# Performance work log

Measured on AMD Instinct MI355X. Metric: run time of the kernel, lower is better.

Reference implementation:

```python
import math
import jax, jax.numpy as jnp
import numpy as np

D_MODEL = 1024
D_FF = 4096
NUM_EXPERTS = 8
TOP_K = 2
CAP_FACTOR = 1.0
AUX_COEF = 0.01
Z_COEF = 0.0


def setup_inputs() -> dict:
    key = jax.random.key(0)
    ks = jax.random.split(key, 6)
    x = jax.random.normal(ks[0], (4, 2048, D_MODEL), dtype=jnp.float32)
    router_w = jax.random.normal(ks[1], (D_MODEL, NUM_EXPERTS), dtype=jnp.float32) / math.sqrt(D_MODEL)
    router_b = jnp.zeros((NUM_EXPERTS,), dtype=jnp.float32)
    w1 = jax.random.normal(ks[2], (NUM_EXPERTS, D_MODEL, D_FF), dtype=jnp.float32) / math.sqrt(D_MODEL)
    w3 = jax.random.normal(ks[3], (NUM_EXPERTS, D_MODEL, D_FF), dtype=jnp.float32) / math.sqrt(D_MODEL)
    w2 = jax.random.normal(ks[4], (NUM_EXPERTS, D_FF, D_MODEL), dtype=jnp.float32) / math.sqrt(D_FF)
    return {"x": x, "router_w": router_w, "router_b": router_b, "w1": w1, "w3": w3, "w2": w2}


def reference(x, router_w, router_b, w1, w3, w2):
    b, s, d = x.shape
    E, k = NUM_EXPERTS, TOP_K
    T = b * s
    x_flat = x.reshape(T, d)

    # ---- router ----
    logits = x_flat @ router_w + router_b                      # [T, E]
    logits_f32 = logits.astype(jnp.float32)
    probs = jax.nn.softmax(logits_f32, axis=-1)                # [T, E]
    topk_p, topk_i = jax.lax.top_k(probs, k)                   # [T, k]
    topk_p = topk_p / jnp.clip(topk_p.sum(-1, keepdims=True), 1e-9)  # normalize_gates
    gate = topk_p.reshape(-1)                                  # [T*k]
    expert_idx = topk_i.reshape(-1)                            # [T*k]

    # ---- aux loss (load balance + z-loss) ----
    importance = probs.mean(axis=0)                            # [E]
    load = jnp.bincount(topk_i[:, 0], length=E).astype(jnp.float32) / T
    lb_loss = (importance * load).sum() * float(E)
    z_loss = jnp.mean(jnp.square(jax.nn.logsumexp(logits_f32, axis=-1)))
    aux_loss = (AUX_COEF * lb_loss + Z_COEF * z_loss).astype(x.dtype)

    # ---- capacity-based dispatch ----
    N = T * k
    cap = max(1, int(math.ceil(CAP_FACTOR * N / E)))
    x_rep = jnp.repeat(x_flat, k, axis=0)                      # [N, d]
    order = jnp.argsort(expert_idx)                            # stable sort by expert
    e_sorted = expert_idx[order]
    x_sorted = x_rep[order]
    g_sorted = gate[order].astype(x.dtype)
    counts = jnp.bincount(e_sorted, length=E)
    starts = jnp.concatenate([jnp.zeros((1,), counts.dtype), jnp.cumsum(counts)[:-1]])
    pos = jnp.arange(N, dtype=counts.dtype) - starts[e_sorted]   # rank within expert group
    keep = pos < cap
    slot = jnp.where(keep, e_sorted * cap + pos, E * cap)      # dropped tokens -> dump row

    buf = jnp.zeros((E * cap + 1, d), dtype=x.dtype).at[slot].set(x_sorted)
    buf = buf[: E * cap].reshape(E, cap, d)                    # [E, C, d]

    # ---- grouped SwiGLU experts ----
    h = jax.nn.silu(jnp.einsum('ecd,edf->ecf', buf, w1)) * jnp.einsum('ecd,edf->ecf', buf, w3)
    y = jnp.einsum('ecf,efd->ecd', h, w2).reshape(E * cap, d)

    # ---- combine ----
    gathered = y[jnp.minimum(slot, E * cap - 1)]
    out_sorted = jnp.where(keep[:, None], gathered, 0.0) * g_sorted[:, None]
    inv = jnp.argsort(order)
    out = out_sorted[inv].reshape(T, k, d).sum(axis=1)
    return out.reshape(b, s, d), aux_loss
```

## Files before the change

### kernel.cpp

```cpp
#include <hip/hip_runtime.h>
#include <hip/hip_bf16.h>
#include <math.h>

constexpr int kT    = 8192;
constexpr int kD    = 1024;
constexpr int kF    = 4096;
constexpr int kE    = 8;
constexpr int kN    = kT * 2;
constexpr int kCap  = 2048;
constexpr int kECap = kE * kCap;

typedef __attribute__((ext_vector_type(8))) short bf16x8;
typedef __attribute__((ext_vector_type(4))) float f32x4;

__device__ __forceinline__ void gload16(const __hip_bfloat16* g, __hip_bfloat16* l) {
  auto gp = (const __attribute__((address_space(1))) __hip_bfloat16*)g;
  auto lp = (__attribute__((address_space(3))) __hip_bfloat16*)l;
  __builtin_amdgcn_global_load_lds((const __attribute__((address_space(1))) void*)gp,
                                   (__attribute__((address_space(3))) void*)lp,
                                   16, 0, 0);
}

#define SYNC_VM(N) do { __builtin_amdgcn_sched_barrier(0); \
  asm volatile("s_waitcnt vmcnt(" #N ")" ::: "memory"); \
  __builtin_amdgcn_s_barrier(); \
  asm volatile("" ::: "memory"); } while (0)

__global__ void init_kernel(int* token_of) {
  int i = blockIdx.x * 256 + threadIdx.x;
  if (i < kECap) token_of[i] = -1;
}

__global__ __launch_bounds__(256)
void transpose64_kernel(const float* __restrict__ srcA, const float* __restrict__ srcB,
                        __hip_bfloat16* __restrict__ dstA, __hip_bfloat16* __restrict__ dstB,
                        int R, int C) {
  __shared__ float tile[64][65];
  const int zz = blockIdx.z;
  const int e = zz & 7;
  const float* src = (zz < 8) ? srcA : srcB;
  __hip_bfloat16* dst = (zz < 8) ? dstA : dstB;
  const size_t mat = (size_t)R * C;
  const float* s = src + (size_t)e * mat;
  __hip_bfloat16* d = dst + (size_t)e * mat;
  const int c0 = blockIdx.x * 64, r0 = blockIdx.y * 64;
  const int tid = threadIdx.x;

  const int lr = tid >> 4, lc4 = (tid & 15) * 4;
#pragma unroll
  for (int p = 0; p < 4; ++p) {
    int r = p * 16 + lr;
    float4 v = *(const float4*)(s + (size_t)(r0 + r) * C + c0 + lc4);
    tile[r][lc4] = v.x; tile[r][lc4 + 1] = v.y; tile[r][lc4 + 2] = v.z; tile[r][lc4 + 3] = v.w;
  }
  __syncthreads();

  const int c = tid >> 2, rc = (tid & 3) * 16;
  union { __hip_bfloat16 h[16]; bf16x8 v[2]; } o;
#pragma unroll
  for (int i = 0; i < 16; ++i) o.h[i] = __float2bfloat16(tile[rc + i][c]);
  __hip_bfloat16* drow = d + (size_t)(c0 + c) * R + r0 + rc;
  *(bf16x8*)drow = o.v[0];
  *(bf16x8*)(drow + 8) = o.v[1];
}

__global__ __launch_bounds__(256)
void router_kernel(const float* __restrict__ x, const float* __restrict__ rw,
                   const float* __restrict__ rb, int* __restrict__ e_idx,
                   float* __restrict__ gates, float* __restrict__ probs_out) {
  int t = blockIdx.x * 4 + (threadIdx.x >> 6);
  int lane = threadIdx.x & 63;
  const float* xr = x + (size_t)t * kD;
  float acc[8];
#pragma unroll
  for (int e = 0; e < 8; ++e) acc[e] = 0.f;
  for (int i = 0; i < kD / 256; ++i) {
    int d = i * 256 + lane * 4;
    float4 xv = *(const float4*)(xr + d);
#pragma unroll
    for (int j = 0; j < 4; ++j) {
      float xs = (j == 0) ? xv.x : (j == 1) ? xv.y : (j == 2) ? xv.z : xv.w;
      const float4* w4 = (const float4*)(rw + (size_t)(d + j) * 8);
      float4 wa = w4[0], wb = w4[1];
      acc[0] += xs * wa.x; acc[1] += xs * wa.y; acc[2] += xs * wa.z; acc[3] += xs * wa.w;
      acc[4] += xs * wb.x; acc[5] += xs * wb.y; acc[6] += xs * wb.z; acc[7] += xs * wb.w;
    }
  }
#pragma unroll
  for (int off = 32; off >= 1; off >>= 1) {
#pragma unroll
    for (int e = 0; e < 8; ++e) acc[e] += __shfl_xor(acc[e], off);
  }
  if (lane == 0) {
    float l[8], m = -1e30f;
#pragma unroll
    for (int e = 0; e < 8; ++e) { l[e] = acc[e] + rb[e]; m = fmaxf(m, l[e]); }
    float p[8], s = 0.f;
#pragma unroll
    for (int e = 0; e < 8; ++e) { p[e] = __expf(l[e] - m); s += p[e]; }
    float inv = 1.f / s;
#pragma unroll
    for (int e = 0; e < 8; ++e) p[e] *= inv;
    int i1 = 0;
#pragma unroll
    for (int e = 1; e < 8; ++e) if (p[e] > p[i1]) i1 = e;
    int i2 = (i1 == 0) ? 1 : 0;
#pragma unroll
    for (int e = 0; e < 8; ++e) if (e != i1 && e != i2 && p[e] > p[i2]) i2 = e;
    float den = fmaxf(p[i1] + p[i2], 1e-9f);
    e_idx[2 * t] = i1; e_idx[2 * t + 1] = i2;
    gates[2 * t] = p[i1] / den; gates[2 * t + 1] = p[i2] / den;
    float4* po = (float4*)(probs_out + (size_t)t * 8);
    po[0] = make_float4(p[0], p[1], p[2], p[3]);
    po[1] = make_float4(p[4], p[5], p[6], p[7]);
  }
}

__global__ __launch_bounds__(1024)
void aux_kernel(const float* __restrict__ probs, const int* __restrict__ e_idx,
                float* __restrict__ aux_out) {
  int tid = threadIdx.x, lane = tid & 63, wave = tid >> 6;
  float imp[8];
  int cnt[8];
#pragma unroll
  for (int e = 0; e < 8; ++e) { imp[e] = 0.f; cnt[e] = 0; }
  for (int t = tid; t < kT; t += 1024) {
    const float4* p4 = (const float4*)(probs + (size_t)t * 8);
    float4 a = p4[0], b = p4[1];
    imp[0] += a.x; imp[1] += a.y; imp[2] += a.z; imp[3] += a.w;
    imp[4] += b.x; imp[5] += b.y; imp[6] += b.z; imp[7] += b.w;
    ++cnt[e_idx[2 * t] & 7];
  }
#pragma unroll
  for (int off = 32; off >= 1; off >>= 1) {
#pragma unroll
    for (int e = 0; e < 8; ++e) {
      imp[e] += __shfl_xor(imp[e], off);
      cnt[e] += __shfl_xor(cnt[e], off);
    }
  }
  __shared__ float simp[16][8];
  __shared__ int scnt[16][8];
  if (lane == 0) {
#pragma unroll
    for (int e = 0; e < 8; ++e) { simp[wave][e] = imp[e]; scnt[wave][e] = cnt[e]; }
  }
  __syncthreads();
  if (tid == 0) {
    float lb = 0.f;
    for (int e = 0; e < 8; ++e) {
      float I = 0.f; int C = 0;
      for (int w = 0; w < 16; ++w) { I += simp[w][e]; C += scnt[w][e]; }
      lb += (I / (float)kT) * ((float)C / (float)kT);
    }
    aux_out[0] = 0.01f * lb * (float)kE;
  }
}

__global__ __launch_bounds__(256)
void rank_kernel(const int* __restrict__ e_idx, int* __restrict__ pos) {
  int e = blockIdx.x;
  __shared__ int wave_sum[4];
  __shared__ int running;
  int tid = threadIdx.x, lane = tid & 63, wave = tid >> 6;
  if (tid == 0) running = 0;
  __syncthreads();
  for (int base = 0; base < kN; base += 256) {
    int i = base + tid;
    bool f = (e_idx[i] == e);
    unsigned long long m = __ballot(f);
    int wpre = __popcll(m & ((1ull << lane) - 1ull));
    if (lane == 0) wave_sum[wave] = __popcll(m);
    __syncthreads();
    int woff = 0;
    for (int w = 0; w < wave; ++w) woff += wave_sum[w];
    int r = running;
    if (f) pos[i] = r + woff + wpre;
    __syncthreads();
    if (tid == 0) running = r + wave_sum[0] + wave_sum[1] + wave_sum[2] + wave_sum[3];
    __syncthreads();
  }
}

__global__ __launch_bounds__(256)
void scatter_kernel(const int* __restrict__ e_idx, const int* __restrict__ pos,
                    int* __restrict__ slot_of, int* __restrict__ token_of) {
  int i = blockIdx.x * 256 + threadIdx.x;
  if (i >= kN) return;
  int p = pos[i];
  if (p < kCap) {
    int slot = e_idx[i] * kCap + p;
    slot_of[i] = slot;
    token_of[slot] = i >> 1;
  } else {
    slot_of[i] = -1;
  }
}

struct __attribute__((aligned(8))) bf16x4s { __hip_bfloat16 v[4]; };

__global__ __launch_bounds__(64)
void gather_kernel(const float* __restrict__ x, const int* __restrict__ token_of,
                   __hip_bfloat16* __restrict__ buf) {
  int slot = blockIdx.x, lane = threadIdx.x;
  int t = token_of[slot];
  __hip_bfloat16* br = buf + (size_t)slot * kD;
  if (t >= 0) {
    const float* xr = x + (size_t)t * kD;
#pragma unroll
    for (int j = 0; j < 4; ++j) {
      int dd = (j * 64 + lane) * 4;
      float4 v = *(const float4*)(xr + dd);
      bf16x4s o;
      o.v[0] = __float2bfloat16(v.x); o.v[1] = __float2bfloat16(v.y);
      o.v[2] = __float2bfloat16(v.z); o.v[3] = __float2bfloat16(v.w);
      *(bf16x4s*)(br + dd) = o;
    }
  } else {
    bf16x4s z;
    z.v[0] = z.v[1] = z.v[2] = z.v[3] = __float2bfloat16(0.f);
#pragma unroll
    for (int j = 0; j < 4; ++j) *(bf16x4s*)(br + (j * 64 + lane) * 4) = z;
  }
}

__global__ __launch_bounds__(512, 2)
void gemm1_kernel(const __hip_bfloat16* __restrict__ Abase,
                  const __hip_bfloat16* __restrict__ W1t,
                  const __hip_bfloat16* __restrict__ W3t,
                  __hip_bfloat16* __restrict__ H) {
  constexpr int K = kD;
  constexpr int NT = K / 64;
  const int e = blockIdx.z, mt = blockIdx.y, ft = blockIdx.x;
  const int tid = threadIdx.x, lane = tid & 63, wave = tid >> 6;
  const int wr = wave >> 1, wc = wave & 1;
  const int frow = lane & 15, fk = lane >> 4;

  const __hip_bfloat16* A  = Abase + (size_t)(e * kCap + mt * 256) * K;
  const __hip_bfloat16* B1 = W1t + ((size_t)e * kF + ft * 128) * K;
  const __hip_bfloat16* B3 = W3t + ((size_t)e * kF + ft * 128) * K;

  extern __shared__ __hip_bfloat16 lds[];

  f32x4 accU[4][4], accV[4][4];
#pragma unroll
  for (int m = 0; m < 4; ++m)
#pragma unroll
    for (int n = 0; n < 4; ++n) {
      accU[m][n] = (f32x4){0.f, 0.f, 0.f, 0.f};
      accV[m][n] = (f32x4){0.f, 0.f, 0.f, 0.f};
    }

  auto stageA = [&](int t, int b) {
#pragma unroll
    for (int j = 0; j < 4; ++j) {
      int c = j * 128 + wc * 64 + lane;
      int rl = c >> 3, s = c & 7;
      const __hip_bfloat16* g = A + (size_t)(wr * 64 + rl) * K + t * 64 + (s ^ (rl & 7)) * 8;
      gload16(g, &lds[b * 32768 + wr * 4096 + (j * 128 + wc * 64) * 8]);
    }
  };
  auto stageB1 = [&](int t, int b) {
#pragma unroll
    for (int j = 0; j < 2; ++j) {
      int c = j * 256 + wr * 64 + lane;
      int rl = c >> 3, s = c & 7;
      const __hip_bfloat16* g = B1 + (size_t)(wc * 64 + rl) * K + t * 64 + (s ^ (rl & 7)) * 8;
      gload16(g, &lds[b * 32768 + 16384 + wc * 4096 + (j * 256 + wr * 64) * 8]);
    }
  };
  auto stageB3 = [&](int t, int b) {
#pragma unroll
    for (int j = 0; j < 2; ++j) {
      int c = j * 256 + wr * 64 + lane;
      int rl = c >> 3, s = c & 7;
      const __hip_bfloat16* g = B3 + (size_t)(wc * 64 + rl) * K + t * 64 + (s ^ (rl & 7)) * 8;
      gload16(g, &lds[b * 32768 + 16384 + 8192 + wc * 4096 + (j * 256 + wr * 64) * 8]);
    }
  };
  auto phase = [&](int b, f32x4 (&ac)[4][4], bf16x8 (&af)[4][2], int broff, bool loadA) {
    if (loadA) {
#pragma unroll
      for (int m = 0; m < 4; ++m)
#pragma unroll
        for (int h = 0; h < 2; ++h) {
          int row = wr * 64 + m * 16 + frow;
          af[m][h] = *(const bf16x8*)&lds[b * 32768 + row * 64 + ((h * 4 + fk) ^ (row & 7)) * 8];
        }
    }
    bf16x8 bf[4][2];
#pragma unroll
    for (int n = 0; n < 4; ++n)
#pragma unroll
      for (int h = 0; h < 2; ++h) {
        int row = broff + wc * 64 + n * 16 + frow;
        bf[n][h] = *(const bf16x8*)&lds[b * 32768 + 16384 + row * 64 + ((h * 4 + fk) ^ (row & 7)) * 8];
      }
    __builtin_amdgcn_s_setprio(1);
#pragma unroll
    for (int m = 0; m < 4; ++m)
#pragma unroll
      for (int n = 0; n < 4; ++n)
#pragma unroll
        for (int h = 0; h < 2; ++h)
          ac[m][n] = __builtin_amdgcn_mfma_f32_16x16x32_bf16(af[m][h], bf[n][h], ac[m][n], 0, 0, 0);
    __builtin_amdgcn_s_setprio(0);
    __builtin_amdgcn_sched_barrier(0);
  };

  stageA(0, 0); stageB1(0, 0); stageB3(0, 0);

  for (int t = 0; t < NT; ++t) {
    const int b = t & 1, nb = b ^ 1;
    const bool nx = (t + 1 < NT);
    SYNC_VM(2);
    if (nx) stageA(t + 1, nb);
    bf16x8 af[4][2];
    phase(b, accU, af, 0, true);
    if (nx) { SYNC_VM(4); } else { SYNC_VM(0); }
    if (nx) stageB1(t + 1, nb);
    phase(b, accV, af, 128, false);
    if (nx) stageB3(t + 1, nb);
  }

  __hip_bfloat16* Ht = H + (size_t)(e * kCap + mt * 256) * kF + ft * 128;
#pragma unroll
  for (int m = 0; m < 4; ++m)
#pragma unroll
    for (int n = 0; n < 4; ++n)
#pragma unroll
      for (int r = 0; r < 4; ++r) {
        int row = wr * 64 + m * 16 + fk * 4 + r;
        int col = wc * 64 + n * 16 + frow;
        float u = accU[m][n][r], v = accV[m][n][r];
        float hval = (u / (1.f + __expf(-u))) * v;
        Ht[(size_t)row * kF + col] = __float2bfloat16(hval);
      }
}

__global__ __launch_bounds__(512, 2)
void gemm2_kernel(const __hip_bfloat16* __restrict__ Hbase,
                  const __hip_bfloat16* __restrict__ W2t,
                  __hip_bfloat16* __restrict__ Y) {
  constexpr int K = kF;
  constexpr int NT = K / 64;
  const int e = blockIdx.z, mt = blockIdx.y, nt = blockIdx.x;
  const int tid = threadIdx.x, lane = tid & 63, wave = tid >> 6;
  const int wr = wave >> 2, wc = wave & 3;
  const int frow = lane & 15, fk = lane >> 4;

  const __hip_bfloat16* A = Hbase + (size_t)(e * kCap + mt * 256) * K;
  const __hip_bfloat16* B = W2t + ((size_t)e * kD + nt * 256) * K;

  extern __shared__ __hip_bfloat16 lds[];

  f32x4 acc[2][4][4];
#pragma unroll
  for (int p = 0; p < 2; ++p)
#pragma unroll
    for (int m = 0; m < 4; ++m)
#pragma unroll
      for (int n = 0; n < 4; ++n) acc[p][m][n] = (f32x4){0.f, 0.f, 0.f, 0.f};

  auto stageB = [&](int t, int b) {
#pragma unroll
    for (int j = 0; j < 4; ++j) {
      int c = j * 128 + wr * 64 + lane;
      int rl = c >> 3, s = c & 7;
      const __hip_bfloat16* g = B + (size_t)(wc * 64 + rl) * K + t * 64 + (s ^ (rl & 7)) * 8;
      gload16(g, &lds[b * 32768 + 16384 + wc * 4096 + (j * 128 + wr * 64) * 8]);
    }
  };
  auto stageA = [&](int t, int p, int b) {
    int q = 2 * wr + p;
#pragma unroll
    for (int j = 0; j < 2; ++j) {
      int c = j * 256 + wc * 64 + lane;
      int rl = c >> 3, s = c & 7;
      const __hip_bfloat16* g = A + (size_t)(q * 64 + rl) * K + t * 64 + (s ^ (rl & 7)) * 8;
      gload16(g, &lds[b * 32768 + q * 4096 + (j * 256 + wc * 64) * 8]);
    }
  };
  auto phase = [&](int b, int p, f32x4 (&ac)[4][4], bf16x8 (&bf)[4][2], bool loadB) {
    bf16x8 a[4][2];
#pragma unroll
    for (int m = 0; m < 4; ++m)
#pragma unroll
      for (int h = 0; h < 2; ++h) {
        int row = wr * 128 + p * 64 + m * 16 + frow;
        a[m][h] = *(const bf16x8*)&lds[b * 32768 + row * 64 + ((h * 4 + fk) ^ (row & 7)) * 8];
      }
    if (loadB) {
#pragma unroll
      for (int n = 0; n < 4; ++n)
#pragma unroll
        for (int h = 0; h < 2; ++h) {
          int row = wc * 64 + n * 16 + frow;
          bf[n][h] = *(const bf16x8*)&lds[b * 32768 + 16384 + row * 64 + ((h * 4 + fk) ^ (row & 7)) * 8];
        }
    }
    __builtin_amdgcn_s_setprio(1);
#pragma unroll
    for (int m = 0; m < 4; ++m)
#pragma unroll
      for (int n = 0; n < 4; ++n)
#pragma unroll
        for (int h = 0; h < 2; ++h)
          ac[m][n] = __builtin_amdgcn_mfma_f32_16x16x32_bf16(a[m][h], bf[n][h], ac[m][n], 0, 0, 0);
    __builtin_amdgcn_s_setprio(0);
    __builtin_amdgcn_sched_barrier(0);
  };

  stageB(0, 0); stageA(0, 0, 0); stageA(0, 1, 0);

  for (int t = 0; t < NT; ++t) {
    const int b = t & 1, nb = b ^ 1;
    const bool nx = (t + 1 < NT);
    SYNC_VM(2);
    if (nx) stageB(t + 1, nb);
    bf16x8 bf[4][2];
    phase(b, 0, acc[0], bf, true);
    if (nx) { SYNC_VM(4); } else { SYNC_VM(0); }
    if (nx) stageA(t + 1, 0, nb);
    phase(b, 1, acc[1], bf, false);
    if (nx) stageA(t + 1, 1, nb);
  }

  __hip_bfloat16* Yt = Y + (size_t)(e * kCap + mt * 256) * kD + nt * 256;
#pragma unroll
  for (int p = 0; p < 2; ++p)
#pragma unroll
    for (int m = 0; m < 4; ++m)
#pragma unroll
      for (int n = 0; n < 4; ++n)
#pragma unroll
        for (int r = 0; r < 4; ++r) {
          int row = wr * 128 + p * 64 + m * 16 + fk * 4 + r;
          int col = wc * 64 + n * 16 + frow;
          Yt[(size_t)row * kD + col] = __float2bfloat16(acc[p][m][n][r]);
        }
}

__global__ __launch_bounds__(256)
void combine_kernel(const __hip_bfloat16* __restrict__ Y, const int* __restrict__ slot_of,
                    const float* __restrict__ gates, float* __restrict__ out) {
  int t = blockIdx.x;
  int dd = threadIdx.x * 4;
  int s0 = slot_of[2 * t], s1 = slot_of[2 * t + 1];
  float g0 = gates[2 * t], g1 = gates[2 * t + 1];
  float4 r = {0.f, 0.f, 0.f, 0.f};
  if (s0 >= 0) {
    bf16x4s v = *(const bf16x4s*)(Y + (size_t)s0 * kD + dd);
    r.x += g0 * __bfloat162float(v.v[0]); r.y += g0 * __bfloat162float(v.v[1]);
    r.z += g0 * __bfloat162float(v.v[2]); r.w += g0 * __bfloat162float(v.v[3]);
  }
  if (s1 >= 0) {
    bf16x4s v = *(const bf16x4s*)(Y + (size_t)s1 * kD + dd);
    r.x += g1 * __bfloat162float(v.v[0]); r.y += g1 * __bfloat162float(v.v[1]);
    r.z += g1 * __bfloat162float(v.v[2]); r.w += g1 * __bfloat162float(v.v[3]);
  }
  *(float4*)(out + (size_t)t * kD + dd) = r;
}

extern "C" void kernel_launch(void* const* d_in, const int* in_sizes, int n_in,
                              void* d_out, int out_size, void* d_ws, size_t ws_size,
                              hipStream_t stream) {
  (void)in_sizes; (void)n_in; (void)out_size; (void)ws_size;
  const float* x  = (const float*)d_in[0];
  const float* rw = (const float*)d_in[1];
  const float* rb = (const float*)d_in[2];
  const float* w1 = (const float*)d_in[3];
  const float* w3 = (const float*)d_in[4];
  const float* w2 = (const float*)d_in[5];
  float* out = (float*)d_out;

  char* base = (char*)d_ws;
  size_t off = 0;
  auto alloc = [&](size_t bytes) -> char* {
    char* r = base + off;
    off += (bytes + 255) & ~(size_t)255;
    return r;
  };
  __hip_bfloat16* w1t = (__hip_bfloat16*)alloc((size_t)kE * kF * kD * 2);
  __hip_bfloat16* w3t = (__hip_bfloat16*)alloc((size_t)kE * kF * kD * 2);
  __hip_bfloat16* w2t = (__hip_bfloat16*)alloc((size_t)kE * kD * kF * 2);
  __hip_bfloat16* buf = (__hip_bfloat16*)alloc((size_t)kECap * kD * 2);
  __hip_bfloat16* h   = (__hip_bfloat16*)alloc((size_t)kECap * kF * 2);
  __hip_bfloat16* y   = (__hip_bfloat16*)alloc((size_t)kECap * kD * 2);
  int*   e_idx    = (int*)alloc((size_t)kN * 4);
  float* gates    = (float*)alloc((size_t)kN * 4);
  int*   pos      = (int*)alloc((size_t)kN * 4);
  int*   slot_of  = (int*)alloc((size_t)kN * 4);
  int*   token_of = (int*)alloc((size_t)kECap * 4);
  float* probs    = (float*)alloc((size_t)kT * 8 * 4);

  init_kernel<<<kECap / 256, 256, 0, stream>>>(token_of);
  router_kernel<<<kT / 4, 256, 0, stream>>>(x, rw, rb, e_idx, gates, probs);
  aux_kernel<<<1, 1024, 0, stream>>>(probs, e_idx, out + (size_t)kT * kD);
  rank_kernel<<<kE, 256, 0, stream>>>(e_idx, pos);
  scatter_kernel<<<kN / 256, 256, 0, stream>>>(e_idx, pos, slot_of, token_of);
  gather_kernel<<<kECap, 64, 0, stream>>>(x, token_of, buf);
  transpose64_kernel<<<dim3(kF / 64, kD / 64, 16), 256, 0, stream>>>(w1, w3, w1t, w3t, kD, kF);
  gemm1_kernel<<<dim3(kF / 128, kCap / 256, kE), 512, 131072, stream>>>(buf, w1t, w3t, h);
  transpose64_kernel<<<dim3(kD / 64, kF / 64, 8), 256, 0, stream>>>(w2, w2, w2t, w2t, kF, kD);
  gemm2_kernel<<<dim3(kD / 256, kCap / 256, kE), 512, 131072, stream>>>(h, w2t, y);
  combine_kernel<<<kT, 256, 0, stream>>>(y, slot_of, gates, out);
}
```

Before: 606.8 us.

## Merge router and weight transposes into one prep kernel; fold scatter into rank

Combines the router and all three weight transpose-and-cast passes into a single launch that dispatches work by block index. The scatter step is folded into the rank kernel, which now writes slot and token maps directly and fills unused capacity slots with -1, so the separate init kernel and pos buffer go away. The goal is fewer launches and less serialization between small kernels, with router work overlapping the bandwidth-heavy transposes. The weight transposes still run on every call, so the main memory traffic is largely unchanged.

```diff
diff --git a/kernel.cpp b/kernel.cpp
--- a/kernel.cpp
+++ b/kernel.cpp
@@ -10,6 +10,10 @@
 constexpr int kCap  = 2048;
 constexpr int kECap = kE * kCap;
 
+constexpr int kRouterBlocks = kT / 4;
+constexpr int kT13Blocks    = (kF / 64) * (kD / 64) * 16;
+constexpr int kT2Blocks     = (kD / 64) * (kF / 64) * 8;
+
 typedef __attribute__((ext_vector_type(8))) short bf16x8;
 typedef __attribute__((ext_vector_type(4))) float f32x4;
 
@@ -26,26 +30,12 @@
   __builtin_amdgcn_s_barrier(); \
   asm volatile("" ::: "memory"); } while (0)
 
-__global__ void init_kernel(int* token_of) {
-  int i = blockIdx.x * 256 + threadIdx.x;
-  if (i < kECap) token_of[i] = -1;
-}
-
-__global__ __launch_bounds__(256)
-void transpose64_kernel(const float* __restrict__ srcA, const float* __restrict__ srcB,
-                        __hip_bfloat16* __restrict__ dstA, __hip_bfloat16* __restrict__ dstB,
-                        int R, int C) {
+__device__ __forceinline__ void transpose_body(const float* __restrict__ s,
+                                               __hip_bfloat16* __restrict__ d,
+                                               int R, int C, int bx, int by) {
   __shared__ float tile[64][65];
-  const int zz = blockIdx.z;
-  const int e = zz & 7;
-  const float* src = (zz < 8) ? srcA : srcB;
-  __hip_bfloat16* dst = (zz < 8) ? dstA : dstB;
-  const size_t mat = (size_t)R * C;
-  const float* s = src + (size_t)e * mat;
-  __hip_bfloat16* d = dst + (size_t)e * mat;
-  const int c0 = blockIdx.x * 64, r0 = blockIdx.y * 64;
+  const int c0 = bx * 64, r0 = by * 64;
   const int tid = threadIdx.x;
-
   const int lr = tid >> 4, lc4 = (tid & 15) * 4;
 #pragma unroll
   for (int p = 0; p < 4; ++p) {
@@ -54,7 +44,6 @@
     tile[r][lc4] = v.x; tile[r][lc4 + 1] = v.y; tile[r][lc4 + 2] = v.z; tile[r][lc4 + 3] = v.w;
   }
   __syncthreads();
-
   const int c = tid >> 2, rc = (tid & 3) * 16;
   union { __hip_bfloat16 h[16]; bf16x8 v[2]; } o;
 #pragma unroll
@@ -65,55 +54,81 @@
 }
 
 __global__ __launch_bounds__(256)
-void router_kernel(const float* __restrict__ x, const float* __restrict__ rw,
-                   const float* __restrict__ rb, int* __restrict__ e_idx,
-                   float* __restrict__ gates, float* __restrict__ probs_out) {
-  int t = blockIdx.x * 4 + (threadIdx.x >> 6);
-  int lane = threadIdx.x & 63;
-  const float* xr = x + (size_t)t * kD;
-  float acc[8];
-#pragma unroll
-  for (int e = 0; e < 8; ++e) acc[e] = 0.f;
-  for (int i = 0; i < kD / 256; ++i) {
-    int d = i * 256 + lane * 4;
-    float4 xv = *(const float4*)(xr + d);
-#pragma unroll
-    for (int j = 0; j < 4; ++j) {
-      float xs = (j == 0) ? xv.x : (j == 1) ? xv.y : (j == 2) ? xv.z : xv.w;
-      const float4* w4 = (const float4*)(rw + (size_t)(d + j) * 8);
-      float4 wa = w4[0], wb = w4[1];
-      acc[0] += xs * wa.x; acc[1] += xs * wa.y; acc[2] += xs * wa.z; acc[3] += xs * wa.w;
-      acc[4] += xs * wb.x; acc[5] += xs * wb.y; acc[6] += xs * wb.z; acc[7] += xs * wb.w;
-    }
-  }
-#pragma unroll
-  for (int off = 32; off >= 1; off >>= 1) {
-#pragma unroll
-    for (int e = 0; e < 8; ++e) acc[e] += __shfl_xor(acc[e], off);
-  }
-  if (lane == 0) {
-    float l[8], m = -1e30f;
-#pragma unroll
-    for (int e = 0; e < 8; ++e) { l[e] = acc[e] + rb[e]; m = fmaxf(m, l[e]); }
-    float p[8], s = 0.f;
-#pragma unroll
-    for (int e = 0; e < 8; ++e) { p[e] = __expf(l[e] - m); s += p[e]; }
-    float inv = 1.f / s;
-#pragma unroll
-    for (int e = 0; e < 8; ++e) p[e] *= inv;
-    int i1 = 0;
-#pragma unroll
-    for (int e = 1; e < 8; ++e) if (p[e] > p[i1]) i1 = e;
-    int i2 = (i1 == 0) ? 1 : 0;
-#pragma unroll
-    for (int e = 0; e < 8; ++e) if (e != i1 && e != i2 && p[e] > p[i2]) i2 = e;
-    float den = fmaxf(p[i1] + p[i2], 1e-9f);
-    e_idx[2 * t] = i1; e_idx[2 * t + 1] = i2;
-    gates[2 * t] = p[i1] / den; gates[2 * t + 1] = p[i2] / den;
-    float4* po = (float4*)(probs_out + (size_t)t * 8);
-    po[0] = make_float4(p[0], p[1], p[2], p[3]);
-    po[1] = make_float4(p[4], p[5], p[6], p[7]);
-  }
+void prep_kernel(const float* __restrict__ x, const float* __restrict__ rw,
+                 const float* __restrict__ rb, int* __restrict__ e_idx,
+                 float* __restrict__ gates, float* __restrict__ probs_out,
+                 const float* __restrict__ w1, const float* __restrict__ w3,
+                 const float* __restrict__ w2, __hip_bfloat16* __restrict__ w1t,
+                 __hip_bfloat16* __restrict__ w3t, __hip_bfloat16* __restrict__ w2t) {
+  int bid = blockIdx.x;
+  if (bid < kRouterBlocks) {
+    int t = bid * 4 + (threadIdx.x >> 6);
+    int lane = threadIdx.x & 63;
+    const float* xr = x + (size_t)t * kD;
+    float acc[8];
+#pragma unroll
+    for (int e = 0; e < 8; ++e) acc[e] = 0.f;
+    for (int i = 0; i < kD / 256; ++i) {
+      int d = i * 256 + lane * 4;
+      float4 xv = *(const float4*)(xr + d);
+#pragma unroll
+      for (int j = 0; j < 4; ++j) {
+        float xs = (j == 0) ? xv.x : (j == 1) ? xv.y : (j == 2) ? xv.z : xv.w;
+        const float4* w4 = (const float4*)(rw + (size_t)(d + j) * 8);
+        float4 wa = w4[0], wb = w4[1];
+        acc[0] += xs * wa.x; acc[1] += xs * wa.y; acc[2] += xs * wa.z; acc[3] += xs * wa.w;
+        acc[4] += xs * wb.x; acc[5] += xs * wb.y; acc[6] += xs * wb.z; acc[7] += xs * wb.w;
+      }
+    }
+#pragma unroll
+    for (int off = 32; off >= 1; off >>= 1) {
+#pragma unroll
+      for (int e = 0; e < 8; ++e) acc[e] += __shfl_xor(acc[e], off);
+    }
+    if (lane == 0) {
+      float l[8], m = -1e30f;
+#pragma unroll
+      for (int e = 0; e < 8; ++e) { l[e] = acc[e] + rb[e]; m = fmaxf(m, l[e]); }
+      float p[8], s = 0.f;
+#pragma unroll
+      for (int e = 0; e < 8; ++e) { p[e] = __expf(l[e] - m); s += p[e]; }
+      float inv = 1.f / s;
+#pragma unroll
+      for (int e = 0; e < 8; ++e) p[e] *= inv;
+      int i1 = 0;
+#pragma unroll
+      for (int e = 1; e < 8; ++e) if (p[e] > p[i1]) i1 = e;
+      int i2 = (i1 == 0) ? 1 : 0;
+#pragma unroll
+      for (int e = 0; e < 8; ++e) if (e != i1 && e != i2 && p[e] > p[i2]) i2 = e;
+      float den = fmaxf(p[i1] + p[i2], 1e-9f);
+      e_idx[2 * t] = i1; e_idx[2 * t + 1] = i2;
+      gates[2 * t] = p[i1] / den; gates[2 * t + 1] = p[i2] / den;
+      float4* po = (float4*)(probs_out + (size_t)t * 8);
+      po[0] = make_float4(p[0], p[1], p[2], p[3]);
+      po[1] = make_float4(p[4], p[5], p[6], p[7]);
+    }
+    return;
+  }
+  const float* src; __hip_bfloat16* dst; int R, C, bx, by;
+  bid -= kRouterBlocks;
+  if (bid < kT13Blocks) {
+    bx = bid & 63; by = (bid >> 6) & 15;
+    int z = bid >> 10;
+    R = kD; C = kF;
+    size_t mat = (size_t)kD * kF;
+    src = ((z < 8) ? w1 : w3) + (size_t)(z & 7) * mat;
+    dst = ((z < 8) ? w1t : w3t) + (size_t)(z & 7) * mat;
+  } else {
+    bid -= kT13Blocks;
+    bx = bid & 15; by = (bid >> 4) & 63;
+    int e2 = bid >> 10;
+    R = kF; C = kD;
+    size_t mat = (size_t)kF * kD;
+    src = w2 + (size_t)e2 * mat;
+    dst = w2t + (size_t)e2 * mat;
+  }
+  transpose_body(src, dst, R, C, bx, by);
 }
 
 __global__ __launch_bounds__(1024)
@@ -158,7 +173,8 @@
 }
 
 __global__ __launch_bounds__(256)
-void rank_kernel(const int* __restrict__ e_idx, int* __restrict__ pos) {
+void rank_kernel(const int* __restrict__ e_idx, int* __restrict__ slot_of,
+                 int* __restrict__ token_of) {
   int e = blockIdx.x;
   __shared__ int wave_sum[4];
   __shared__ int running;
@@ -175,26 +191,21 @@
     int woff = 0;
     for (int w = 0; w < wave; ++w) woff += wave_sum[w];
     int r = running;
-    if (f) pos[i] = r + woff + wpre;
+    if (f) {
+      int p = r + woff + wpre;
+      if (p < kCap) {
+        slot_of[i] = e * kCap + p;
+        token_of[e * kCap + p] = i >> 1;
+      } else {
+        slot_of[i] = -1;
+      }
+    }
     __syncthreads();
     if (tid == 0) running = r + wave_sum[0] + wave_sum[1] + wave_sum[2] + wave_sum[3];
     __syncthreads();
   }
-}
-
-__global__ __launch_bounds__(256)
-void scatter_kernel(const int* __restrict__ e_idx, const int* __restrict__ pos,
-                    int* __restrict__ slot_of, int* __restrict__ token_of) {
-  int i = blockIdx.x * 256 + threadIdx.x;
-  if (i >= kN) return;
-  int p = pos[i];
-  if (p < kCap) {
-    int slot = e_idx[i] * kCap + p;
-    slot_of[i] = slot;
-    token_of[slot] = i >> 1;
-  } else {
-    slot_of[i] = -1;
-  }
+  for (int p = running + tid; p < kCap; p += 256)
+    token_of[e * kCap + p] = -1;
 }
 
 struct __attribute__((aligned(8))) bf16x4s { __hip_bfloat16 v[4]; };
@@ -489,20 +500,16 @@
   __hip_bfloat16* y   = (__hip_bfloat16*)alloc((size_t)kECap * kD * 2);
   int*   e_idx    = (int*)alloc((size_t)kN * 4);
   float* gates    = (float*)alloc((size_t)kN * 4);
-  int*   pos      = (int*)alloc((size_t)kN * 4);
   int*   slot_of  = (int*)alloc((size_t)kN * 4);
   int*   token_of = (int*)alloc((size_t)kECap * 4);
   float* probs    = (float*)alloc((size_t)kT * 8 * 4);
 
-  init_kernel<<<kECap / 256, 256, 0, stream>>>(token_of);
-  router_kernel<<<kT / 4, 256, 0, stream>>>(x, rw, rb, e_idx, gates, probs);
+  prep_kernel<<<kRouterBlocks + kT13Blocks + kT2Blocks, 256, 0, stream>>>(
+      x, rw, rb, e_idx, gates, probs, w1, w3, w2, w1t, w3t, w2t);
   aux_kernel<<<1, 1024, 0, stream>>>(probs, e_idx, out + (size_t)kT * kD);
-  rank_kernel<<<kE, 256, 0, stream>>>(e_idx, pos);
-  scatter_kernel<<<kN / 256, 256, 0, stream>>>(e_idx, pos, slot_of, token_of);
+  rank_kernel<<<kE, 256, 0, stream>>>(e_idx, slot_of, token_of);
   gather_kernel<<<kECap, 64, 0, stream>>>(x, token_of, buf);
-  transpose64_kernel<<<dim3(kF / 64, kD / 64, 16), 256, 0, stream>>>(w1, w3, w1t, w3t, kD, kF);
   gemm1_kernel<<<dim3(kF / 128, kCap / 256, kE), 512, 131072, stream>>>(buf, w1t, w3t, h);
-  transpose64_kernel<<<dim3(kD / 64, kF / 64, 8), 256, 0, stream>>>(w2, w2, w2t, w2t, kF, kD);
   gemm2_kernel<<<dim3(kD / 256, kCap / 256, kE), 512, 131072, stream>>>(h, w2t, y);
   combine_kernel<<<kT, 256, 0, stream>>>(y, slot_of, gates, out);
 }
```

Result: no change. 602.1 us, median of 2 (-0.8%).
